# Kernel tuning notes

Measured on AMD Instinct MI355X. Metric: run time of the kernel, lower is better.

Reference implementation:

```python
import jax, jax.numpy as jnp
import numpy as np

R_CUT = 10.0
ROUNDS = 1  # num_message_passing_rounds


def setup_inputs() -> dict:
    key = jax.random.key(0)
    N, DEG, S, NRBF, G = 10000, 16, 128, 20, 64
    E = N * DEG
    ks = jax.random.split(key, 16)
    w = lambda k, shp, fan: (jax.random.normal(k, shp, dtype=jnp.float32) / np.float32(np.sqrt(fan)))
    return {
        "edge_vector_diffs": jax.random.normal(ks[0], (E, 3), dtype=jnp.float32) * 3.0,
        "edge_lengths": jax.random.uniform(ks[1], (E,), dtype=jnp.float32) * 15.0,
        "node_from": jnp.repeat(jnp.arange(N), DEG),            # every node has DEG outgoing edges
        "node_graph_index": jax.random.randint(ks[2], (N,), 0, G),
        "num_graphs": G,
        "emb0": jax.random.normal(ks[3], (S,), dtype=jnp.float32) * 0.01,  # embedding.weight[0]
        "phi_w1": w(ks[4], (S, S), S), "phi_b1": jnp.zeros((S,), jnp.float32),
        "phi_w2": w(ks[5], (S, 3 * S), S), "phi_b2": jnp.zeros((3 * S,), jnp.float32),
        "filt_w": w(ks[6], (NRBF, 3 * S), NRBF), "filt_b": jnp.zeros((3 * S,), jnp.float32),
        "u_w": w(ks[7], (S, S), S), "v_w": w(ks[8], (S, S), S),
        "upd_w1": w(ks[9], (2 * S, S), 2 * S), "upd_b1": jnp.zeros((S,), jnp.float32),
        "upd_w2": w(ks[10], (S, 3 * S), S), "upd_b2": jnp.zeros((3 * S,), jnp.float32),
        "out_w1": w(ks[11], (S, S), S), "out_b1": jnp.zeros((S,), jnp.float32),
        "out_w2": w(ks[12], (S, 1), S), "out_b2": jnp.zeros((1,), jnp.float32),
    }


def reference(edge_vector_diffs, edge_lengths, node_from, node_graph_index, num_graphs,
              emb0, phi_w1, phi_b1, phi_w2, phi_b2, filt_w, filt_b, u_w, v_w,
              upd_w1, upd_b1, upd_w2, upd_b2, out_w1, out_b1, out_w2, out_b2):
    S = phi_w1.shape[0]
    N = node_graph_index.shape[0]
    NRBF = filt_w.shape[0]
    silu = jax.nn.silu
    seg = lambda v, n: jax.ops.segment_sum(v, node_from, num_segments=n)

    mask = (jnp.abs(edge_lengths) <= R_CUT).astype(jnp.float32)          # [E] nbr_mask
    r = jnp.linalg.norm(edge_vector_diffs, axis=1)                        # [E]
    r_safe = jnp.maximum(r, 1e-12)
    k = jnp.arange(1, NRBF + 1, dtype=jnp.float32)
    # PAINN sinc radial basis sin(k*pi*r/r_cut)/r, then linear -> [E, 3S]
    rbf = jnp.sin(k[None, :] * jnp.pi * r_safe[:, None] / R_CUT) / r_safe[:, None]
    cutoff = 0.5 * (jnp.cos(jnp.pi * r / R_CUT) + 1.0) * (r < R_CUT)      # cosine cutoff
    W = (rbf @ filt_w + filt_b) * cutoff[:, None]                          # [E, 3S]

    tile3 = jnp.arange(S) % 3  # xyzxyz... truncation pattern from .repeat(...)[: S]
    # scalar Frobenius norm of each node's masked neighbor-diff block
    frob = jnp.sqrt(seg(mask * r * r, N))                                  # [N]
    denom_e = frob[node_from]
    denom_e = jnp.where(denom_e > 0, denom_e, 1.0)
    normalized = edge_vector_diffs / denom_e[:, None]                      # [E, 3]
    norm_exp = normalized[:, tile3]                                        # [E, S]

    # state init: sum over dim 1 of embedding(zeros) == S * embedding.weight[0]
    state = jnp.broadcast_to(jnp.float32(S) * emb0, (N, S))
    state_vec = jnp.zeros((N, 3, S), jnp.float32)

    for _ in range(ROUNDS):
        # message block (nbrs_node_from == destination node, so sync update == original sequential loop)
        phi = silu(state[node_from] @ phi_w1 + phi_b1) @ phi_w2 + phi_b2   # [E, 3S]
        prod = phi * W
        m1, m2, m3 = prod[:, :S], prod[:, S:2 * S], prod[:, 2 * S:]
        vec_msg = state_vec[node_from] * m1[:, None, :] + (norm_exp * m3)[:, None, :]  # [E,3,S]
        state = seg(m2 * mask[:, None], N)                                 # [N, S]
        state_vec = seg(vec_msg * mask[:, None, None], N)                  # [N, 3, S]
        # update block
        U = jnp.einsum('nps,st->npt', state_vec, u_w)                      # [N,3,S]
        V = jnp.einsum('nps,st->npt', state_vec, v_w)
        UV = jnp.einsum('nps,nqs->npq', U, V)                              # [N,3,3]
        Vnorm = jnp.sqrt(jnp.sum(V * V, axis=1))                           # [N,S]
        a = silu(jnp.concatenate([Vnorm, state], axis=-1) @ upd_w1 + upd_b1) @ upd_w2 + upd_b2
        a_vv, a_sv, a_ss = a[:, :S], a[:, S:2 * S], a[:, 2 * S:]
        uv_tiled = jnp.sum(UV, axis=1)[:, tile3]                           # [N,S]
        state = a_ss + uv_tiled * a_sv
        state_vec = U * a_vv[:, None, :]

    graph_state = jax.ops.segment_sum(state, node_graph_index, num_segments=num_graphs)
    out = (silu(graph_state @ out_w1 + out_b1) @ out_w2 + out_b2).ravel()  # [num_graphs]
    return out
```

## Files before the change

### kernel.cpp

```cpp
#include <hip/hip_runtime.h>
#include <math.h>

#define NN   10000
#define DEG  16
#define SS   128
#define NRBF 20
#define GG   64
#define RC   10.0f
#define PI_F 3.14159265358979323846f
#define NBK  8
#define PADN 10

__device__ __forceinline__ float silu_f(float x){
    return x / (1.0f + __expf(-x));
}

__global__ __launch_bounds__(128) void k_phi(
    const float* __restrict__ emb0,
    const float* __restrict__ w1, const float* __restrict__ b1,
    const float* __restrict__ w2, const float* __restrict__ b2,
    float* __restrict__ phiW, float* __restrict__ gs){
    __shared__ float s0[SS];
    __shared__ float hL[SS];
    __shared__ float part[4][32];
    int t = threadIdx.x;
    for (int i = blockIdx.x*128 + t; i < GG*SS; i += 12*128) gs[i] = 0.0f;
    s0[t] = 128.0f * emb0[t];
    __syncthreads();
    float acc = b1[t];
    #pragma unroll 4
    for (int s = 0; s < SS; s++) acc = fmaf(s0[s], w1[s*SS + t], acc);
    hL[t] = silu_f(acc);
    __syncthreads();
    int c  = blockIdx.x*32 + (t & 31);
    int kk = t >> 5;
    float a = 0.0f;
    int sbase = kk * 32;
    #pragma unroll 8
    for (int s = 0; s < 32; s++)
        a = fmaf(hL[sbase + s], w2[(sbase + s)*3*SS + c], a);
    part[kk][t & 31] = a;
    __syncthreads();
    if (t < 32){
        int cc = blockIdx.x*32 + t;
        phiW[cc] = b2[cc] + part[0][t] + part[1][t] + part[2][t] + part[3][t];
    }
}

__global__ __launch_bounds__(128) void k_fused(
    const float* __restrict__ evd, const float* __restrict__ elen,
    const int* __restrict__ ngi,
    const float* __restrict__ filt_w, const float* __restrict__ filt_b,
    const float* __restrict__ phiW,
    const float* __restrict__ u_w, const float* __restrict__ v_w,
    const float* __restrict__ upd_w1, const float* __restrict__ upd_b1,
    const float* __restrict__ upd_w2, const float* __restrict__ upd_b2,
    float* __restrict__ gs){
    __shared__ float  rbfL[NBK*DEG*NRBF];
    __shared__ float4 edgeS[NBK*DEG];
    __shared__ float  frS[NBK*DEG];
    __shared__ float  svT[SS*PADN];
    __shared__ float  xT[2*SS*PADN];
    __shared__ float  invD[NBK];
    __shared__ float  dL[NBK];
    __shared__ int    gIdx[NBK];

    int t  = threadIdx.x;
    int nb = blockIdx.x * NBK;

    {
        int e = nb*DEG + t;
        float x = evd[3*e+0], y = evd[3*e+1], z = evd[3*e+2];
        float r = sqrtf(x*x + y*y + z*z);
        float len  = elen[e];
        float mask = (fabsf(len) <= RC) ? 1.0f : 0.0f;
        float cut  = (r < RC) ? 0.5f*(__cosf(PI_F*(1.0f/RC)*r) + 1.0f) : 0.0f;
        float mc   = mask * cut;
        float rs   = fmaxf(r, 1e-12f);
        frS[t]   = mask * r * r;
        edgeS[t] = make_float4(mc, x, y, z);
        float inv_rs = 1.0f / rs;
        float base   = (PI_F/RC) * rs;
        float rb[NRBF];
        #pragma unroll
        for (int k = 0; k < NRBF; k++)
            rb[k] = __sinf(base * (float)(k+1)) * inv_rs;
        float4* dst = (float4*)(rbfL + t*NRBF);
        dst[0] = make_float4(rb[0],rb[1],rb[2],rb[3]);
        dst[1] = make_float4(rb[4],rb[5],rb[6],rb[7]);
        dst[2] = make_float4(rb[8],rb[9],rb[10],rb[11]);
        dst[3] = make_float4(rb[12],rb[13],rb[14],rb[15]);
        dst[4] = make_float4(rb[16],rb[17],rb[18],rb[19]);
    }
    __syncthreads();
    if (t < NBK){
        float s = 0.0f;
        #pragma unroll
        for (int e = 0; e < DEG; e++) s += frS[t*DEG + e];
        float fb = sqrtf(s);
        invD[t] = (fb > 0.0f) ? 1.0f/fb : 1.0f;
        gIdx[t] = ngi[nb + t];
    }
    __syncthreads();
    {
        float4 es = edgeS[t];
        float f = es.x * invD[t >> 4];
        edgeS[t] = make_float4(es.x, es.y*f, es.z*f, es.w*f);
    }
    __syncthreads();

    {
        int wv = t >> 6, l = t & 63;
        int gcA = SS + l, gcB = SS + 64 + l;
        int gcC = 2*SS + l, gcD = 2*SS + 64 + l;
        float fwA[NRBF], fwB[NRBF], fwC[NRBF], fwD[NRBF];
        #pragma unroll
        for (int k = 0; k < NRBF; k++){
            fwA[k] = filt_w[k*(3*SS) + gcA];
            fwB[k] = filt_w[k*(3*SS) + gcB];
            fwC[k] = filt_w[k*(3*SS) + gcC];
            fwD[k] = filt_w[k*(3*SS) + gcD];
        }
        float fbA = filt_b[gcA], fbB = filt_b[gcB];
        float fbC = filt_b[gcC], fbD = filt_b[gcD];
        float phA = phiW[gcA], phB = phiW[gcB];
        float phC = phiW[gcC], phD = phiW[gcD];
        int s3C = l % 3, s3D = (l + 64) % 3;

        for (int ni = 0; ni < 4; ni++){
            int node = 4*wv + ni;
            float accA = 0.f, accB = 0.f, accC = 0.f, accD = 0.f;
            #pragma unroll 4
            for (int e = 0; e < DEG; e++){
                int eg = node*DEG + e;
                const float4* rv = (const float4*)(rbfL + eg*NRBF);
                float4 r0 = rv[0], r1 = rv[1], r2 = rv[2], r3 = rv[3], r4 = rv[4];
                float rr[NRBF] = {r0.x,r0.y,r0.z,r0.w, r1.x,r1.y,r1.z,r1.w,
                                  r2.x,r2.y,r2.z,r2.w, r3.x,r3.y,r3.z,r3.w,
                                  r4.x,r4.y,r4.z,r4.w};
                float4 es = edgeS[eg];
                float wA = fbA, wB = fbB, wC = fbC, wD = fbD;
                #pragma unroll
                for (int k = 0; k < NRBF; k++){
                    wA = fmaf(rr[k], fwA[k], wA);
                    wB = fmaf(rr[k], fwB[k], wB);
                    wC = fmaf(rr[k], fwC[k], wC);
                    wD = fmaf(rr[k], fwD[k], wD);
                }
                float fC = (s3C == 0) ? es.y : ((s3C == 1) ? es.z : es.w);
                float fD = (s3D == 0) ? es.y : ((s3D == 1) ? es.z : es.w);
                accA = fmaf(phA*es.x, wA, accA);
                accB = fmaf(phB*es.x, wB, accB);
                accC = fmaf(phC*fC,  wC, accC);
                accD = fmaf(phD*fD,  wD, accD);
            }
            xT[(SS + l)*PADN + node]      = accA;
            xT[(SS + 64 + l)*PADN + node] = accB;
            svT[l*PADN + node]            = accC;
            svT[(64 + l)*PADN + node]     = accD;
        }
    }
    __syncthreads();

    int cg = t & 31, ng = t >> 5;
    int c0 = 4*cg, n0 = 2*ng;

    float accU[4][2], accV[4][2];
    #pragma unroll
    for (int j = 0; j < 4; j++){
        accU[j][0] = accU[j][1] = 0.f;
        accV[j][0] = accV[j][1] = 0.f;
    }
    #pragma unroll 4
    for (int k = 0; k < SS; k++){
        float2 xv = *(const float2*)(svT + k*PADN + n0);
        float4 wu = *(const float4*)(u_w + k*SS + c0);
        float4 wv4 = *(const float4*)(v_w + k*SS + c0);
        float wua[4] = {wu.x, wu.y, wu.z, wu.w};
        float wva[4] = {wv4.x, wv4.y, wv4.z, wv4.w};
        #pragma unroll
        for (int j = 0; j < 4; j++){
            accU[j][0] = fmaf(xv.x, wua[j], accU[j][0]);
            accU[j][1] = fmaf(xv.y, wua[j], accU[j][1]);
            accV[j][0] = fmaf(xv.x, wva[j], accV[j][0]);
            accV[j][1] = fmaf(xv.y, wva[j], accV[j][1]);
        }
    }
    float pd0 = 0.f, pd1 = 0.f;
    #pragma unroll
    for (int j = 0; j < 4; j++){
        pd0 = fmaf(accU[j][0], accV[j][0], pd0);
        pd1 = fmaf(accU[j][1], accV[j][1], pd1);
    }
    #pragma unroll
    for (int m = 1; m <= 16; m <<= 1){
        pd0 += __shfl_xor(pd0, m);
        pd1 += __shfl_xor(pd1, m);
    }
    if (cg == 0){ dL[n0] = pd0; dL[n0+1] = pd1; }
    const float SQ3 = 1.7320508075688772f;
    #pragma unroll
    for (int j = 0; j < 4; j++){
        xT[(c0+j)*PADN + n0]     = SQ3 * fabsf(accV[j][0]);
        xT[(c0+j)*PADN + n0 + 1] = SQ3 * fabsf(accV[j][1]);
    }
    __syncthreads();
    float d30 = 3.0f*dL[n0], d31 = 3.0f*dL[n0+1];

    float accH[4][2];
    #pragma unroll
    for (int j = 0; j < 4; j++) accH[j][0] = accH[j][1] = 0.f;
    #pragma unroll 4
    for (int k = 0; k < 2*SS; k++){
        float2 xv = *(const float2*)(xT + k*PADN + n0);
        float4 w4 = *(const float4*)(upd_w1 + k*SS + c0);
        float wa[4] = {w4.x, w4.y, w4.z, w4.w};
        #pragma unroll
        for (int j = 0; j < 4; j++){
            accH[j][0] = fmaf(xv.x, wa[j], accH[j][0]);
            accH[j][1] = fmaf(xv.y, wa[j], accH[j][1]);
        }
    }
    {
        float4 b1v = *(const float4*)(upd_b1 + c0);
        float ba[4] = {b1v.x, b1v.y, b1v.z, b1v.w};
        #pragma unroll
        for (int j = 0; j < 4; j++){
            svT[(c0+j)*PADN + n0]     = silu_f(accH[j][0] + ba[j]);
            svT[(c0+j)*PADN + n0 + 1] = silu_f(accH[j][1] + ba[j]);
        }
    }
    __syncthreads();

    float a2[4][2], a3[4][2];
    #pragma unroll
    for (int j = 0; j < 4; j++){
        a2[j][0] = a2[j][1] = 0.f;
        a3[j][0] = a3[j][1] = 0.f;
    }
    #pragma unroll 4
    for (int k = 0; k < SS; k++){
        float2 hx = *(const float2*)(svT + k*PADN + n0);
        float4 w2 = *(const float4*)(upd_w2 + k*3*SS + SS   + c0);
        float4 w3 = *(const float4*)(upd_w2 + k*3*SS + 2*SS + c0);
        float w2a[4] = {w2.x, w2.y, w2.z, w2.w};
        float w3a[4] = {w3.x, w3.y, w3.z, w3.w};
        #pragma unroll
        for (int j = 0; j < 4; j++){
            a2[j][0] = fmaf(hx.x, w2a[j], a2[j][0]);
            a2[j][1] = fmaf(hx.y, w2a[j], a2[j][1]);
            a3[j][0] = fmaf(hx.x, w3a[j], a3[j][0]);
            a3[j][1] = fmaf(hx.y, w3a[j], a3[j][1]);
        }
    }
    float4 bsv4 = *(const float4*)(upd_b2 + SS   + c0);
    float4 bss4 = *(const float4*)(upd_b2 + 2*SS + c0);
    float bsv[4] = {bsv4.x, bsv4.y, bsv4.z, bsv4.w};
    float bss[4] = {bss4.x, bss4.y, bss4.z, bss4.w};
    int g0 = gIdx[n0], g1 = gIdx[n0+1];
    #pragma unroll
    for (int j = 0; j < 4; j++){
        float ns0 = (a3[j][0] + bss[j]) + d30*(a2[j][0] + bsv[j]);
        float ns1 = (a3[j][1] + bss[j]) + d31*(a2[j][1] + bsv[j]);
        atomicAdd(&gs[g0*SS + c0 + j], ns0);
        atomicAdd(&gs[g1*SS + c0 + j], ns1);
    }
}

__global__ __launch_bounds__(128) void k_out(
    const float* __restrict__ gs,
    const float* __restrict__ w1, const float* __restrict__ b1,
    const float* __restrict__ w2, const float* __restrict__ b2,
    float* __restrict__ out){
    __shared__ float gsL[SS];
    __shared__ float red[2];
    int g = blockIdx.x, t = threadIdx.x;
    gsL[t] = gs[g*SS + t];
    __syncthreads();
    float acc = b1[t];
    #pragma unroll 4
    for (int s = 0; s < SS; s++) acc = fmaf(gsL[s], w1[s*SS + t], acc);
    float p = silu_f(acc) * w2[t];
    for (int off = 32; off; off >>= 1) p += __shfl_down(p, off);
    if ((t & 63) == 0) red[t >> 6] = p;
    __syncthreads();
    if (t == 0) out[g] = red[0] + red[1] + b2[0];
}

extern "C" void kernel_launch(void* const* d_in, const int* in_sizes, int n_in,
                              void* d_out, int out_size, void* d_ws, size_t ws_size,
                              hipStream_t stream) {
    const float* evd     = (const float*)d_in[0];
    const float* elen    = (const float*)d_in[1];
    const int*   ngi     = (const int*)  d_in[3];
    const float* emb0    = (const float*)d_in[5];
    const float* phi_w1  = (const float*)d_in[6];
    const float* phi_b1  = (const float*)d_in[7];
    const float* phi_w2  = (const float*)d_in[8];
    const float* phi_b2  = (const float*)d_in[9];
    const float* filt_w  = (const float*)d_in[10];
    const float* filt_b  = (const float*)d_in[11];
    const float* u_w     = (const float*)d_in[12];
    const float* v_w     = (const float*)d_in[13];
    const float* upd_w1  = (const float*)d_in[14];
    const float* upd_b1  = (const float*)d_in[15];
    const float* upd_w2  = (const float*)d_in[16];
    const float* upd_b2  = (const float*)d_in[17];
    const float* out_w1  = (const float*)d_in[18];
    const float* out_b1  = (const float*)d_in[19];
    const float* out_w2  = (const float*)d_in[20];
    const float* out_b2  = (const float*)d_in[21];

    float* ws   = (float*)d_ws;
    float* phiW = ws;
    float* gs   = ws + 512;

    k_phi<<<12, 128, 0, stream>>>(emb0, phi_w1, phi_b1, phi_w2, phi_b2, phiW, gs);
    k_fused<<<NN/NBK, 128, 0, stream>>>(evd, elen, ngi, filt_w, filt_b, phiW,
                                        u_w, v_w, upd_w1, upd_b1, upd_w2, upd_b2, gs);
    k_out<<<GG, 128, 0, stream>>>(gs, out_w1, out_b1, out_w2, out_b2, (float*)d_out);
}
```

Measured before the change: 201.0 us.

## Pre-reduce radial basis over edges before filter projection, double nodes per block

The filter is linear in the radial basis, so each 16-edge group now sums the basis terms weighted by cutoff and by the cutoff-scaled direction vector using wave shuffles. The filter weights are then applied once per node instead of once per edge. This removes most of the per-edge FMA work and the shared-memory rbf staging, along with a sync-heavy normalisation pass. The block now covers 16 nodes with 256 threads and a launch-bounds occupancy hint. The shuffle reductions and the larger register load may limit occupancy.

```diff
diff --git a/kernel.cpp b/kernel.cpp
--- a/kernel.cpp
+++ b/kernel.cpp
@@ -8,8 +8,9 @@
 #define GG   64
 #define RC   10.0f
 #define PI_F 3.14159265358979323846f
-#define NBK  8
-#define PADN 10
+#define NBK  16
+#define PADN 18
+#define SARR 88
 
 __device__ __forceinline__ float silu_f(float x){
     return x / (1.0f + __expf(-x));
@@ -47,7 +48,7 @@
     }
 }
 
-__global__ __launch_bounds__(128) void k_fused(
+__global__ __launch_bounds__(256, 4) void k_fused(
     const float* __restrict__ evd, const float* __restrict__ elen,
     const int* __restrict__ ngi,
     const float* __restrict__ filt_w, const float* __restrict__ filt_b,
@@ -56,20 +57,19 @@
     const float* __restrict__ upd_w1, const float* __restrict__ upd_b1,
     const float* __restrict__ upd_w2, const float* __restrict__ upd_b2,
     float* __restrict__ gs){
-    __shared__ float  rbfL[NBK*DEG*NRBF];
-    __shared__ float4 edgeS[NBK*DEG];
-    __shared__ float  frS[NBK*DEG];
-    __shared__ float  svT[SS*PADN];
-    __shared__ float  xT[2*SS*PADN];
-    __shared__ float  invD[NBK];
-    __shared__ float  dL[NBK];
-    __shared__ int    gIdx[NBK];
+    __shared__ float sArr[NBK*SARR];
+    __shared__ float svT[SS*PADN];
+    __shared__ float xT[2*SS*PADN];
+    __shared__ float dL[NBK];
+    __shared__ int   gIdx[NBK];
 
     int t  = threadIdx.x;
     int nb = blockIdx.x * NBK;
+    if (t < NBK) gIdx[t] = ngi[nb + t];
 
     {
-        int e = nb*DEG + t;
+        int e  = nb*DEG + t;
+        int el = t & 15;
         float x = evd[3*e+0], y = evd[3*e+1], z = evd[3*e+2];
         float r = sqrtf(x*x + y*y + z*z);
         float len  = elen[e];
@@ -77,41 +77,60 @@
         float cut  = (r < RC) ? 0.5f*(__cosf(PI_F*(1.0f/RC)*r) + 1.0f) : 0.0f;
         float mc   = mask * cut;
         float rs   = fmaxf(r, 1e-12f);
-        frS[t]   = mask * r * r;
-        edgeS[t] = make_float4(mc, x, y, z);
         float inv_rs = 1.0f / rs;
         float base   = (PI_F/RC) * rs;
-        float rb[NRBF];
-        #pragma unroll
-        for (int k = 0; k < NRBF; k++)
-            rb[k] = __sinf(base * (float)(k+1)) * inv_rs;
-        float4* dst = (float4*)(rbfL + t*NRBF);
-        dst[0] = make_float4(rb[0],rb[1],rb[2],rb[3]);
-        dst[1] = make_float4(rb[4],rb[5],rb[6],rb[7]);
-        dst[2] = make_float4(rb[8],rb[9],rb[10],rb[11]);
-        dst[3] = make_float4(rb[12],rb[13],rb[14],rb[15]);
-        dst[4] = make_float4(rb[16],rb[17],rb[18],rb[19]);
-    }
-    __syncthreads();
-    if (t < NBK){
-        float s = 0.0f;
-        #pragma unroll
-        for (int e = 0; e < DEG; e++) s += frS[t*DEG + e];
-        float fb = sqrtf(s);
-        invD[t] = (fb > 0.0f) ? 1.0f/fb : 1.0f;
-        gIdx[t] = ngi[nb + t];
-    }
-    __syncthreads();
-    {
-        float4 es = edgeS[t];
-        float f = es.x * invD[t >> 4];
-        edgeS[t] = make_float4(es.x, es.y*f, es.z*f, es.w*f);
+        float px = mc*x, py = mc*y, pz = mc*z;
+        float fr = mask * r * r;
+
+        float* sa = sArr + (t >> 4)*SARR;
+
+        {
+            float a0 = mc, a1 = px, a2 = py, a3 = pz, a4 = fr;
+            #pragma unroll
+            for (int m = 1; m <= 8; m <<= 1){
+                a0 += __shfl_xor(a0, m, 16);
+                a1 += __shfl_xor(a1, m, 16);
+                a2 += __shfl_xor(a2, m, 16);
+                a3 += __shfl_xor(a3, m, 16);
+                a4 += __shfl_xor(a4, m, 16);
+            }
+            if (el == 0) sa[80] = a0;
+            if (el == 1) sa[81] = a1;
+            if (el == 2) sa[82] = a2;
+            if (el == 3) sa[83] = a3;
+            if (el == 4) sa[84] = (a4 > 0.0f) ? (1.0f/sqrtf(a4)) : 1.0f;
+        }
+
+        #pragma unroll
+        for (int kc = 0; kc < 5; kc++){
+            float ql[16];
+            #pragma unroll
+            for (int kk = 0; kk < 4; kk++){
+                int k = kc*4 + kk;
+                float rb = __sinf(base * (float)(k+1)) * inv_rs;
+                ql[0*4 + kk]  = mc * rb;
+                ql[1*4 + kk]  = px * rb;
+                ql[2*4 + kk]  = py * rb;
+                ql[3*4 + kk]  = pz * rb;
+            }
+            #pragma unroll
+            for (int m = 1; m <= 8; m <<= 1){
+                #pragma unroll
+                for (int i = 0; i < 16; i++)
+                    ql[i] += __shfl_xor(ql[i], m, 16);
+            }
+            float val = ql[0];
+            #pragma unroll
+            for (int j = 1; j < 16; j++)
+                val = (el == j) ? ql[j] : val;
+            sa[(el >> 2)*20 + kc*4 + (el & 3)] = val;
+        }
     }
     __syncthreads();
 
     {
         int wv = t >> 6, l = t & 63;
-        int gcA = SS + l, gcB = SS + 64 + l;
+        int gcA = SS + l,   gcB = SS + 64 + l;
         int gcC = 2*SS + l, gcD = 2*SS + 64 + l;
         float fwA[NRBF], fwB[NRBF], fwC[NRBF], fwD[NRBF];
         #pragma unroll
@@ -127,37 +146,34 @@
         float phC = phiW[gcC], phD = phiW[gcD];
         int s3C = l % 3, s3D = (l + 64) % 3;
 
+        #pragma unroll
         for (int ni = 0; ni < 4; ni++){
             int node = 4*wv + ni;
-            float accA = 0.f, accB = 0.f, accC = 0.f, accD = 0.f;
-            #pragma unroll 4
-            for (int e = 0; e < DEG; e++){
-                int eg = node*DEG + e;
-                const float4* rv = (const float4*)(rbfL + eg*NRBF);
-                float4 r0 = rv[0], r1 = rv[1], r2 = rv[2], r3 = rv[3], r4 = rv[4];
-                float rr[NRBF] = {r0.x,r0.y,r0.z,r0.w, r1.x,r1.y,r1.z,r1.w,
-                                  r2.x,r2.y,r2.z,r2.w, r3.x,r3.y,r3.z,r3.w,
-                                  r4.x,r4.y,r4.z,r4.w};
-                float4 es = edgeS[eg];
-                float wA = fbA, wB = fbB, wC = fbC, wD = fbD;
-                #pragma unroll
-                for (int k = 0; k < NRBF; k++){
-                    wA = fmaf(rr[k], fwA[k], wA);
-                    wB = fmaf(rr[k], fwB[k], wB);
-                    wC = fmaf(rr[k], fwC[k], wC);
-                    wD = fmaf(rr[k], fwD[k], wD);
-                }
-                float fC = (s3C == 0) ? es.y : ((s3C == 1) ? es.z : es.w);
-                float fD = (s3D == 0) ? es.y : ((s3D == 1) ? es.z : es.w);
-                accA = fmaf(phA*es.x, wA, accA);
-                accB = fmaf(phB*es.x, wB, accB);
-                accC = fmaf(phC*fC,  wC, accC);
-                accD = fmaf(phD*fD,  wD, accD);
+            const float* sa = sArr + node*SARR;
+            float M   = sa[80];
+            float t0C = sa[81 + s3C], t0D = sa[81 + s3D];
+            float iD  = sa[84];
+            float dA = fbA*M,   dB = fbB*M;
+            float dC = fbC*t0C, dD = fbD*t0D;
+            #pragma unroll
+            for (int kc = 0; kc < 5; kc++){
+                float4 s2 = *(const float4*)(sa + kc*4);
+                float4 tc = *(const float4*)(sa + (1+s3C)*20 + kc*4);
+                float4 td = *(const float4*)(sa + (1+s3D)*20 + kc*4);
+                int k = kc*4;
+                dA = fmaf(s2.x, fwA[k], dA); dA = fmaf(s2.y, fwA[k+1], dA);
+                dA = fmaf(s2.z, fwA[k+2], dA); dA = fmaf(s2.w, fwA[k+3], dA);
+                dB = fmaf(s2.x, fwB[k], dB); dB = fmaf(s2.y, fwB[k+1], dB);
+                dB = fmaf(s2.z, fwB[k+2], dB); dB = fmaf(s2.w, fwB[k+3], dB);
+                dC = fmaf(tc.x, fwC[k], dC); dC = fmaf(tc.y, fwC[k+1], dC);
+                dC = fmaf(tc.z, fwC[k+2], dC); dC = fmaf(tc.w, fwC[k+3], dC);
+                dD = fmaf(td.x, fwD[k], dD); dD = fmaf(td.y, fwD[k+1], dD);
+                dD = fmaf(td.z, fwD[k+2], dD); dD = fmaf(td.w, fwD[k+3], dD);
             }
-            xT[(SS + l)*PADN + node]      = accA;
-            xT[(SS + 64 + l)*PADN + node] = accB;
-            svT[l*PADN + node]            = accC;
-            svT[(64 + l)*PADN + node]     = accD;
+            xT[(SS + l)*PADN + node]      = phA * dA;
+            xT[(SS + 64 + l)*PADN + node] = phB * dB;
+            svT[l*PADN + node]            = phC * iD * dC;
+            svT[(64 + l)*PADN + node]     = phD * iD * dD;
         }
     }
     __syncthreads();
@@ -316,7 +332,7 @@
     float* gs   = ws + 512;
 
     k_phi<<<12, 128, 0, stream>>>(emb0, phi_w1, phi_b1, phi_w2, phi_b2, phiW, gs);
-    k_fused<<<NN/NBK, 128, 0, stream>>>(evd, elen, ngi, filt_w, filt_b, phiW,
+    k_fused<<<NN/NBK, 256, 0, stream>>>(evd, elen, ngi, filt_w, filt_b, phiW,
                                         u_w, v_w, upd_w1, upd_b1, upd_w2, upd_b2, gs);
     k_out<<<GG, 128, 0, stream>>>(gs, out_w1, out_b1, out_w2, out_b2, (float*)d_out);
 }
```

Result: slower. 205.6 us (+2.3%).

## Fuse phi, main, and output kernels into one launch with last-block readout

Applied to the files above, without the earlier changes.

Folds the three kernels into a single kernel. Every block recomputes the phi MLP into shared memory, which removes the separate phi launch. The last block to finish, detected with an atomic counter, runs the output MLP over the graph sums. A memset now zeroes the accumulator and counter. This saves two kernel launches and their dependency gaps, at the cost of redundant phi work in every one of the 1250 blocks (two 128-wide matvecs each) and a serialized tail done by one block.

```diff
diff --git a/kernel.cpp b/kernel.cpp
--- a/kernel.cpp
+++ b/kernel.cpp
@@ -10,52 +10,28 @@
 #define PI_F 3.14159265358979323846f
 #define NBK  8
 #define PADN 10
+#define NBLK (NN/NBK)
 
 __device__ __forceinline__ float silu_f(float x){
     return x / (1.0f + __expf(-x));
 }
 
-__global__ __launch_bounds__(128) void k_phi(
-    const float* __restrict__ emb0,
-    const float* __restrict__ w1, const float* __restrict__ b1,
-    const float* __restrict__ w2, const float* __restrict__ b2,
-    float* __restrict__ phiW, float* __restrict__ gs){
-    __shared__ float s0[SS];
-    __shared__ float hL[SS];
-    __shared__ float part[4][32];
-    int t = threadIdx.x;
-    for (int i = blockIdx.x*128 + t; i < GG*SS; i += 12*128) gs[i] = 0.0f;
-    s0[t] = 128.0f * emb0[t];
-    __syncthreads();
-    float acc = b1[t];
-    #pragma unroll 4
-    for (int s = 0; s < SS; s++) acc = fmaf(s0[s], w1[s*SS + t], acc);
-    hL[t] = silu_f(acc);
-    __syncthreads();
-    int c  = blockIdx.x*32 + (t & 31);
-    int kk = t >> 5;
-    float a = 0.0f;
-    int sbase = kk * 32;
-    #pragma unroll 8
-    for (int s = 0; s < 32; s++)
-        a = fmaf(hL[sbase + s], w2[(sbase + s)*3*SS + c], a);
-    part[kk][t & 31] = a;
-    __syncthreads();
-    if (t < 32){
-        int cc = blockIdx.x*32 + t;
-        phiW[cc] = b2[cc] + part[0][t] + part[1][t] + part[2][t] + part[3][t];
-    }
-}
-
-__global__ __launch_bounds__(128) void k_fused(
+__global__ __launch_bounds__(128) void k_all(
     const float* __restrict__ evd, const float* __restrict__ elen,
     const int* __restrict__ ngi,
+    const float* __restrict__ emb0,
+    const float* __restrict__ phi_w1, const float* __restrict__ phi_b1,
+    const float* __restrict__ phi_w2, const float* __restrict__ phi_b2,
     const float* __restrict__ filt_w, const float* __restrict__ filt_b,
-    const float* __restrict__ phiW,
     const float* __restrict__ u_w, const float* __restrict__ v_w,
     const float* __restrict__ upd_w1, const float* __restrict__ upd_b1,
     const float* __restrict__ upd_w2, const float* __restrict__ upd_b2,
-    float* __restrict__ gs){
+    const float* __restrict__ out_w1, const float* __restrict__ out_b1,
+    const float* __restrict__ out_w2, const float* __restrict__ out_b2,
+    float* __restrict__ gs, unsigned int* __restrict__ counter,
+    float* __restrict__ out){
+    __shared__ float  phW[3*SS];
+    __shared__ float  hL[SS];
     __shared__ float  rbfL[NBK*DEG*NRBF];
     __shared__ float4 edgeS[NBK*DEG];
     __shared__ float  frS[NBK*DEG];
@@ -64,9 +40,34 @@
     __shared__ float  invD[NBK];
     __shared__ float  dL[NBK];
     __shared__ int    gIdx[NBK];
+    __shared__ float  gRow[2][SS];
+    __shared__ int    lastFlag;
 
     int t  = threadIdx.x;
     int nb = blockIdx.x * NBK;
+
+    frS[t] = 128.0f * emb0[t];
+    __syncthreads();
+    {
+        float acc = phi_b1[t];
+        #pragma unroll 4
+        for (int s = 0; s < SS; s++) acc = fmaf(frS[s], phi_w1[s*SS + t], acc);
+        hL[t] = silu_f(acc);
+    }
+    __syncthreads();
+    {
+        float a0 = phi_b2[t], a1 = phi_b2[SS + t], a2 = phi_b2[2*SS + t];
+        #pragma unroll 4
+        for (int s = 0; s < SS; s++){
+            float hv = hL[s];
+            const float* row = phi_w2 + s*3*SS;
+            a0 = fmaf(hv, row[t],        a0);
+            a1 = fmaf(hv, row[SS + t],   a1);
+            a2 = fmaf(hv, row[2*SS + t], a2);
+        }
+        phW[t] = a0; phW[SS + t] = a1; phW[2*SS + t] = a2;
+    }
+    __syncthreads();
 
     {
         int e = nb*DEG + t;
@@ -123,8 +124,8 @@
         }
         float fbA = filt_b[gcA], fbB = filt_b[gcB];
         float fbC = filt_b[gcC], fbD = filt_b[gcD];
-        float phA = phiW[gcA], phB = phiW[gcB];
-        float phC = phiW[gcC], phD = phiW[gcD];
+        float phA = phW[gcA], phB = phW[gcB];
+        float phC = phW[gcC], phD = phW[gcD];
         int s3C = l % 3, s3D = (l + 64) % 3;
 
         for (int ni = 0; ni < 4; ni++){
@@ -253,38 +254,60 @@
             a3[j][1] = fmaf(hx.y, w3a[j], a3[j][1]);
         }
     }
-    float4 bsv4 = *(const float4*)(upd_b2 + SS   + c0);
-    float4 bss4 = *(const float4*)(upd_b2 + 2*SS + c0);
-    float bsv[4] = {bsv4.x, bsv4.y, bsv4.z, bsv4.w};
-    float bss[4] = {bss4.x, bss4.y, bss4.z, bss4.w};
-    int g0 = gIdx[n0], g1 = gIdx[n0+1];
-    #pragma unroll
-    for (int j = 0; j < 4; j++){
-        float ns0 = (a3[j][0] + bss[j]) + d30*(a2[j][0] + bsv[j]);
-        float ns1 = (a3[j][1] + bss[j]) + d31*(a2[j][1] + bsv[j]);
-        atomicAdd(&gs[g0*SS + c0 + j], ns0);
-        atomicAdd(&gs[g1*SS + c0 + j], ns1);
-    }
-}
-
-__global__ __launch_bounds__(128) void k_out(
-    const float* __restrict__ gs,
-    const float* __restrict__ w1, const float* __restrict__ b1,
-    const float* __restrict__ w2, const float* __restrict__ b2,
-    float* __restrict__ out){
-    __shared__ float gsL[SS];
-    __shared__ float red[2];
-    int g = blockIdx.x, t = threadIdx.x;
-    gsL[t] = gs[g*SS + t];
-    __syncthreads();
-    float acc = b1[t];
-    #pragma unroll 4
-    for (int s = 0; s < SS; s++) acc = fmaf(gsL[s], w1[s*SS + t], acc);
-    float p = silu_f(acc) * w2[t];
-    for (int off = 32; off; off >>= 1) p += __shfl_down(p, off);
-    if ((t & 63) == 0) red[t >> 6] = p;
-    __syncthreads();
-    if (t == 0) out[g] = red[0] + red[1] + b2[0];
+    {
+        float4 bsv4 = *(const float4*)(upd_b2 + SS   + c0);
+        float4 bss4 = *(const float4*)(upd_b2 + 2*SS + c0);
+        float bsv[4] = {bsv4.x, bsv4.y, bsv4.z, bsv4.w};
+        float bss[4] = {bss4.x, bss4.y, bss4.z, bss4.w};
+        int g0 = gIdx[n0], g1 = gIdx[n0+1];
+        #pragma unroll
+        for (int j = 0; j < 4; j++){
+            float ns0 = (a3[j][0] + bss[j]) + d30*(a2[j][0] + bsv[j]);
+            float ns1 = (a3[j][1] + bss[j]) + d31*(a2[j][1] + bsv[j]);
+            atomicAdd(&gs[g0*SS + c0 + j], ns0);
+            atomicAdd(&gs[g1*SS + c0 + j], ns1);
+        }
+    }
+
+    __threadfence();
+    if (t == 0){
+        unsigned int v = atomicAdd(counter, 1u);
+        lastFlag = (v == (unsigned int)(NBLK - 1)) ? 1 : 0;
+    }
+    __syncthreads();
+    if (lastFlag){
+        __threadfence();
+        int wv = t >> 6, l = t & 63;
+        int cc0 = 2*l;
+        float2 ob1 = *(const float2*)(out_b1 + cc0);
+        float2 ow2 = *(const float2*)(out_w2 + cc0);
+        float  ob2 = out_b2[0];
+        for (int g = wv; g < GG; g += 2){
+            gRow[wv][l]      = __hip_atomic_load(gs + g*SS + l,
+                                  __ATOMIC_RELAXED, __HIP_MEMORY_SCOPE_AGENT);
+            gRow[wv][64 + l] = __hip_atomic_load(gs + g*SS + 64 + l,
+                                  __ATOMIC_RELAXED, __HIP_MEMORY_SCOPE_AGENT);
+            __syncthreads();
+            float acc0 = ob1.x, acc1 = ob1.y;
+            #pragma unroll 4
+            for (int s4 = 0; s4 < SS; s4 += 4){
+                float4 gv = *(const float4*)(&gRow[wv][s4]);
+                float2 w0 = *(const float2*)(out_w1 + (s4+0)*SS + cc0);
+                float2 w1 = *(const float2*)(out_w1 + (s4+1)*SS + cc0);
+                float2 w2 = *(const float2*)(out_w1 + (s4+2)*SS + cc0);
+                float2 w3 = *(const float2*)(out_w1 + (s4+3)*SS + cc0);
+                acc0 = fmaf(gv.x, w0.x, acc0); acc1 = fmaf(gv.x, w0.y, acc1);
+                acc0 = fmaf(gv.y, w1.x, acc0); acc1 = fmaf(gv.y, w1.y, acc1);
+                acc0 = fmaf(gv.z, w2.x, acc0); acc1 = fmaf(gv.z, w2.y, acc1);
+                acc0 = fmaf(gv.w, w3.x, acc0); acc1 = fmaf(gv.w, w3.y, acc1);
+            }
+            float p = silu_f(acc0)*ow2.x + silu_f(acc1)*ow2.y;
+            #pragma unroll
+            for (int off = 32; off; off >>= 1) p += __shfl_down(p, off);
+            if (l == 0) out[g] = p + ob2;
+            __syncthreads();
+        }
+    }
 }
 
 extern "C" void kernel_launch(void* const* d_in, const int* in_sizes, int n_in,
@@ -311,12 +334,15 @@
     const float* out_w2  = (const float*)d_in[20];
     const float* out_b2  = (const float*)d_in[21];
 
-    float* ws   = (float*)d_ws;
-    float* phiW = ws;
-    float* gs   = ws + 512;
-
-    k_phi<<<12, 128, 0, stream>>>(emb0, phi_w1, phi_b1, phi_w2, phi_b2, phiW, gs);
-    k_fused<<<NN/NBK, 128, 0, stream>>>(evd, elen, ngi, filt_w, filt_b, phiW,
-                                        u_w, v_w, upd_w1, upd_b1, upd_w2, upd_b2, gs);
-    k_out<<<GG, 128, 0, stream>>>(gs, out_w1, out_b1, out_w2, out_b2, (float*)d_out);
+    float*        ws      = (float*)d_ws;
+    float*        gs      = ws;
+    unsigned int* counter = (unsigned int*)(ws + GG*SS);
+
+    hipMemsetAsync(d_ws, 0, (GG*SS + 16)*sizeof(float), stream);
+    k_all<<<NBLK, 128, 0, stream>>>(evd, elen, ngi, emb0,
+                                    phi_w1, phi_b1, phi_w2, phi_b2,
+                                    filt_w, filt_b, u_w, v_w,
+                                    upd_w1, upd_b1, upd_w2, upd_b2,
+                                    out_w1, out_b1, out_w2, out_b2,
+                                    gs, counter, (float*)d_out);
 }
```

After: 312.7 us. +55.6%, slower.
